# Kernel optimization log

Hardware: AMD Instinct MI355X
Metric: run time of the kernel (lower is better)

The kernel has to match this reference:

```python
import jax, jax.numpy as jnp
import numpy as np

B, H, S, D = 2, 16, 2048, 64
SOFTCLAMP = 50.0


def setup_inputs() -> dict:
    key = jax.random.key(0)
    kq, kk, kv, km = jax.random.split(key, 4)
    q = jax.random.normal(kq, (B, H, S, D), dtype=jnp.float32)
    k = jax.random.normal(kk, (B, H, S, D), dtype=jnp.float32)
    v = jax.random.normal(kv, (B, H, S, D), dtype=jnp.float32)
    mask = jax.random.randint(km, (B, S), 0, 2).astype(jnp.bool_)
    return {"q": q, "k": k, "v": v, "mask": mask}


def reference(q, k, v, mask):
    scale = q.shape[-1] ** -0.5
    # [b, h, i, j] similarity logits
    sim = jnp.einsum('bhid,bhjd->bhij', q, k) * scale
    # tanh-based logit softclamping (Gemma2-style softcapping)
    sim = jnp.tanh(sim / SOFTCLAMP) * SOFTCLAMP
    mask_value = -jnp.finfo(sim.dtype).max
    sim = jnp.where(mask[:, None, None, :], sim, mask_value)
    attn = jax.nn.softmax(sim, axis=-1)
    out = jnp.einsum('bhij,bhjd->bhid', attn, v)
    return out, attn
```

## Files before the change

### kernel.cpp

```cpp
#include <hip/hip_runtime.h>
#include <hip/hip_bf16.h>

#define B_ 2
#define H_ 16
#define S_ 2048
#define D_ 64
#define PSTR 2056

typedef float f32x4 __attribute__((ext_vector_type(4)));
typedef short s16x8 __attribute__((ext_vector_type(8)));

__device__ __forceinline__ short f2bf(float f) {
  unsigned u = __float_as_uint(f);
  u += 0x7FFFu + ((u >> 16) & 1u);
  return (short)(u >> 16);
}
__device__ __forceinline__ float bf2f(short s) {
  return __uint_as_float(((unsigned)(unsigned short)s) << 16);
}

__global__ __launch_bounds__(256) void prep_qk(const float* __restrict__ q,
                                               const float* __restrict__ k,
                                               short* __restrict__ qbf,
                                               short* __restrict__ kbf) {
  size_t i = ((size_t)blockIdx.x * 256 + threadIdx.x) * 8;
  const f32x4* qa = (const f32x4*)(q + i);
  const f32x4* ka = (const f32x4*)(k + i);
  f32x4 a0 = __builtin_nontemporal_load(qa);
  f32x4 a1 = __builtin_nontemporal_load(qa + 1);
  f32x4 b0 = __builtin_nontemporal_load(ka);
  f32x4 b1 = __builtin_nontemporal_load(ka + 1);
  s16x8 oq, ok;
  #pragma unroll
  for (int e = 0; e < 4; ++e) {
    oq[e] = f2bf(a0[e]); oq[4 + e] = f2bf(a1[e]);
    ok[e] = f2bf(b0[e]); ok[4 + e] = f2bf(b1[e]);
  }
  *(s16x8*)(qbf + i) = oq;
  *(s16x8*)(kbf + i) = ok;
}

__global__ __launch_bounds__(256) void prep_v(const float* __restrict__ v,
                                              short* __restrict__ vt) {
  __shared__ float tile[64][65];
  const int tid = threadIdx.x;
  const int j0 = blockIdx.x * 64;
  const int bh = blockIdx.y;
  const float* vh = v + (size_t)bh * S_ * D_;
  #pragma unroll
  for (int it = 0; it < 16; ++it) {
    int idx = it * 256 + tid;
    int row = idx >> 6, col = idx & 63;
    tile[row][col] = __builtin_nontemporal_load(&vh[(size_t)(j0 + row) * D_ + col]);
  }
  __syncthreads();
  short* vth = vt + (size_t)bh * D_ * S_;
  #pragma unroll
  for (int it = 0; it < 16; ++it) {
    int idx = it * 256 + tid;
    int d = idx >> 6, jj = idx & 63;
    vth[(size_t)d * S_ + j0 + jj] = f2bf(tile[jj][d]);
  }
}

template <bool PRE>
__global__ __launch_bounds__(512, 4) void attend_kernel(
    const float* __restrict__ q, const float* __restrict__ k,
    const float* __restrict__ v, const int* __restrict__ mask,
    const short* __restrict__ qbf, const short* __restrict__ kbf,
    const short* __restrict__ vt,
    float* __restrict__ out, float* __restrict__ attn) {
  __shared__ short ps[16 * PSTR];
  __shared__ float ls_rs[8][16];
  __shared__ float ls_rinv[16];

  const int tid  = threadIdx.x;
  const int wv   = tid >> 6;
  const int lane = tid & 63;
  const int lg   = lane >> 4;
  const int li   = lane & 15;

  const int q0 = blockIdx.x * 16;
  const int bh = blockIdx.y;
  const int b  = bh >> 4;
  const int* mrow = mask + (size_t)b * S_;

  s16x8 qf[2];
  if constexpr (PRE) {
    const short* qr = qbf + ((size_t)bh * S_ + q0 + li) * D_ + lg * 8;
    qf[0] = *(const s16x8*)qr;
    qf[1] = *(const s16x8*)(qr + 32);
  } else {
    const float* qr = q + ((size_t)bh * S_ + q0 + li) * D_ + lg * 8;
    #pragma unroll
    for (int ks = 0; ks < 2; ++ks)
      #pragma unroll
      for (int e = 0; e < 8; ++e) qf[ks][e] = f2bf(qr[ks * 32 + e]);
  }

  float rs[4] = {0.f, 0.f, 0.f, 0.f};

  for (int c = wv; c < S_ / 64; c += 8) {
    const int jc = c * 64;
    f32x4 acc[4];
    #pragma unroll
    for (int n = 0; n < 4; ++n) acc[n] = (f32x4){0.f, 0.f, 0.f, 0.f};

    #pragma unroll
    for (int n = 0; n < 4; ++n) {
      if constexpr (PRE) {
        const short* kr = kbf + ((size_t)bh * S_ + jc + n * 16 + li) * D_ + lg * 8;
        acc[n] = __builtin_amdgcn_mfma_f32_16x16x32_bf16(qf[0], *(const s16x8*)kr, acc[n], 0, 0, 0);
        acc[n] = __builtin_amdgcn_mfma_f32_16x16x32_bf16(qf[1], *(const s16x8*)(kr + 32), acc[n], 0, 0, 0);
      } else {
        const float* kr = k + ((size_t)bh * S_ + jc + n * 16 + li) * D_ + lg * 8;
        s16x8 kf0, kf1;
        #pragma unroll
        for (int e = 0; e < 8; ++e) { kf0[e] = f2bf(kr[e]); kf1[e] = f2bf(kr[32 + e]); }
        acc[n] = __builtin_amdgcn_mfma_f32_16x16x32_bf16(qf[0], kf0, acc[n], 0, 0, 0);
        acc[n] = __builtin_amdgcn_mfma_f32_16x16x32_bf16(qf[1], kf1, acc[n], 0, 0, 0);
      }
    }

    #pragma unroll
    for (int n = 0; n < 4; ++n) {
      const int j = jc + n * 16 + li;
      const bool keep = mrow[j] != 0;
      #pragma unroll
      for (int r = 0; r < 4; ++r) {
        float s = acc[n][r] * 0.125f;
        float t = exp2f(s * 0.057707802f);
        float p = exp2f(-144.269504f * __builtin_amdgcn_rcpf(t + 1.f));
        p = keep ? p : 0.f;
        rs[r] += p;
        ps[(lg * 4 + r) * PSTR + j] = f2bf(p);
      }
    }
  }

  #pragma unroll
  for (int r = 0; r < 4; ++r) {
    #pragma unroll
    for (int m = 1; m < 16; m <<= 1) rs[r] += __shfl_xor(rs[r], m, 64);
  }
  if (li == 0) {
    #pragma unroll
    for (int r = 0; r < 4; ++r) ls_rs[wv][lg * 4 + r] = rs[r];
  }
  __syncthreads();
  if (tid < 16) {
    float ssum = 0.f;
    #pragma unroll
    for (int w = 0; w < 8; ++w) ssum += ls_rs[w][tid];
    ls_rinv[tid] = (ssum > 0.f) ? 1.f / ssum : 0.f;
  }
  __syncthreads();

  if (wv < 4) {
    float* abase = attn + ((size_t)bh * S_ + q0) * S_;
    #pragma unroll 4
    for (int qq = 0; qq < 16; ++qq) {
      const float ri = ls_rinv[qq];
      s16x8 pv = *(const s16x8*)&ps[qq * PSTR + tid * 8];
      f32x4 a0, a1;
      a0[0] = bf2f(pv[0]) * ri; a0[1] = bf2f(pv[1]) * ri;
      a0[2] = bf2f(pv[2]) * ri; a0[3] = bf2f(pv[3]) * ri;
      a1[0] = bf2f(pv[4]) * ri; a1[1] = bf2f(pv[5]) * ri;
      a1[2] = bf2f(pv[6]) * ri; a1[3] = bf2f(pv[7]) * ri;
      f32x4* ap = (f32x4*)(abase + (size_t)qq * S_ + tid * 8);
      __builtin_nontemporal_store(a0, ap);
      __builtin_nontemporal_store(a1, ap + 1);
    }
  } else {
    const int d0 = (wv - 4) * 16;
    f32x4 oa = (f32x4){0.f, 0.f, 0.f, 0.f};
    f32x4 ob = (f32x4){0.f, 0.f, 0.f, 0.f};
    if constexpr (PRE) {
      const short* vrow = vt + ((size_t)bh * D_ + d0 + li) * S_;
      #pragma unroll 2
      for (int jc = 0; jc < S_; jc += 64) {
        s16x8 pa0 = *(const s16x8*)&ps[li * PSTR + jc + lg * 8];
        s16x8 pa1 = *(const s16x8*)&ps[li * PSTR + jc + 32 + lg * 8];
        s16x8 vb0 = *(const s16x8*)(vrow + jc + lg * 8);
        s16x8 vb1 = *(const s16x8*)(vrow + jc + 32 + lg * 8);
        oa = __builtin_amdgcn_mfma_f32_16x16x32_bf16(pa0, vb0, oa, 0, 0, 0);
        ob = __builtin_amdgcn_mfma_f32_16x16x32_bf16(pa1, vb1, ob, 0, 0, 0);
      }
    } else {
      const float* vp0 = v + (size_t)bh * S_ * D_ + d0 + li;
      for (int jc = 0; jc < S_; jc += 32) {
        s16x8 pa = *(const s16x8*)&ps[li * PSTR + jc + lg * 8];
        s16x8 vb;
        const float* vp = vp0 + (size_t)(jc + lg * 8) * D_;
        #pragma unroll
        for (int e = 0; e < 8; ++e) vb[e] = f2bf(vp[(size_t)e * D_]);
        oa = __builtin_amdgcn_mfma_f32_16x16x32_bf16(pa, vb, oa, 0, 0, 0);
      }
    }
    #pragma unroll
    for (int r = 0; r < 4; ++r) {
      const int qq = lg * 4 + r;
      out[((size_t)bh * S_ + q0 + qq) * D_ + d0 + li] = (oa[r] + ob[r]) * ls_rinv[qq];
    }
  }
}

extern "C" void kernel_launch(void* const* d_in, const int* in_sizes, int n_in,
                              void* d_out, int out_size, void* d_ws, size_t ws_size,
                              hipStream_t stream) {
  const float* q = (const float*)d_in[0];
  const float* k = (const float*)d_in[1];
  const float* v = (const float*)d_in[2];
  const int* mask = (const int*)d_in[3];

  float* out  = (float*)d_out;
  const size_t nel = (size_t)B_ * H_ * S_ * D_;
  float* attn = out + nel;

  dim3 grid(S_ / 16, B_ * H_);
  const size_t need = nel * 2 * 3;

  if (ws_size >= need) {
    short* qbf = (short*)d_ws;
    short* kbf = qbf + nel;
    short* vtp = kbf + nel;
    prep_qk<<<(int)(nel / (256 * 8)), 256, 0, stream>>>(q, k, qbf, kbf);
    prep_v<<<dim3(S_ / 64, B_ * H_), 256, 0, stream>>>(v, vtp);
    attend_kernel<true><<<grid, 512, 0, stream>>>(q, k, v, mask, qbf, kbf, vtp, out, attn);
  } else {
    attend_kernel<false><<<grid, 512, 0, stream>>>(q, k, v, mask, nullptr, nullptr, nullptr, out, attn);
  }
}
```

Baseline: 332.5 us.

## Fuse PV matmul into the QK loop with per-wave LDS buffers and register-held probabilities

Each wave now computes P·V for its own 64-key chunks right after the softmax numerators, using a small per-wave LDS staging buffer instead of a full 16x2048 probability tile. Partial outputs are reduced across waves through LDS. Probabilities are kept packed in registers and written to attn after normalization, so all 8 waves share the store work. This cuts LDS use to raise occupancy and spreads the attn writes and PV work evenly, at the cost of more registers and a cross-wave reduction. The attn stores are now scalar and strided per lane rather than vectorized.

```diff
diff --git a/kernel.cpp b/kernel.cpp
--- a/kernel.cpp
+++ b/kernel.cpp
@@ -5,7 +5,8 @@
 #define H_ 16
 #define S_ 2048
 #define D_ 64
-#define PSTR 2056
+#define BUFSTR 72
+#define BUFSZ (16 * BUFSTR)
 
 typedef float f32x4 __attribute__((ext_vector_type(4)));
 typedef short s16x8 __attribute__((ext_vector_type(8)));
@@ -64,13 +65,13 @@
 }
 
 template <bool PRE>
-__global__ __launch_bounds__(512, 4) void attend_kernel(
+__global__ __launch_bounds__(512, 4) void attend_fused(
     const float* __restrict__ q, const float* __restrict__ k,
     const float* __restrict__ v, const int* __restrict__ mask,
     const short* __restrict__ qbf, const short* __restrict__ kbf,
     const short* __restrict__ vt,
     float* __restrict__ out, float* __restrict__ attn) {
-  __shared__ short ps[16 * PSTR];
+  __shared__ float pvred[8][16][64];
   __shared__ float ls_rs[8][16];
   __shared__ float ls_rinv[16];
 
@@ -85,40 +86,45 @@
   const int b  = bh >> 4;
   const int* mrow = mask + (size_t)b * S_;
 
-  s16x8 qf[2];
+  short* myb = (short*)pvred + wv * BUFSZ;
+
+  s16x8 qf0, qf1;
   if constexpr (PRE) {
     const short* qr = qbf + ((size_t)bh * S_ + q0 + li) * D_ + lg * 8;
-    qf[0] = *(const s16x8*)qr;
-    qf[1] = *(const s16x8*)(qr + 32);
+    qf0 = *(const s16x8*)qr;
+    qf1 = *(const s16x8*)(qr + 32);
   } else {
     const float* qr = q + ((size_t)bh * S_ + q0 + li) * D_ + lg * 8;
     #pragma unroll
-    for (int ks = 0; ks < 2; ++ks)
-      #pragma unroll
-      for (int e = 0; e < 8; ++e) qf[ks][e] = f2bf(qr[ks * 32 + e]);
+    for (int e = 0; e < 8; ++e) { qf0[e] = f2bf(qr[e]); qf1[e] = f2bf(qr[32 + e]); }
   }
 
   float rs[4] = {0.f, 0.f, 0.f, 0.f};
-
-  for (int c = wv; c < S_ / 64; c += 8) {
-    const int jc = c * 64;
+  f32x4 pvacc[4];
+  #pragma unroll
+  for (int m = 0; m < 4; ++m) pvacc[m] = (f32x4){0.f, 0.f, 0.f, 0.f};
+  unsigned st[4][4][2];
+
+  #pragma unroll
+  for (int c = 0; c < 4; ++c) {
+    const int jc = c * 512 + wv * 64;
+
     f32x4 acc[4];
     #pragma unroll
     for (int n = 0; n < 4; ++n) acc[n] = (f32x4){0.f, 0.f, 0.f, 0.f};
-
     #pragma unroll
     for (int n = 0; n < 4; ++n) {
       if constexpr (PRE) {
         const short* kr = kbf + ((size_t)bh * S_ + jc + n * 16 + li) * D_ + lg * 8;
-        acc[n] = __builtin_amdgcn_mfma_f32_16x16x32_bf16(qf[0], *(const s16x8*)kr, acc[n], 0, 0, 0);
-        acc[n] = __builtin_amdgcn_mfma_f32_16x16x32_bf16(qf[1], *(const s16x8*)(kr + 32), acc[n], 0, 0, 0);
+        acc[n] = __builtin_amdgcn_mfma_f32_16x16x32_bf16(qf0, *(const s16x8*)kr, acc[n], 0, 0, 0);
+        acc[n] = __builtin_amdgcn_mfma_f32_16x16x32_bf16(qf1, *(const s16x8*)(kr + 32), acc[n], 0, 0, 0);
       } else {
         const float* kr = k + ((size_t)bh * S_ + jc + n * 16 + li) * D_ + lg * 8;
-        s16x8 kf0, kf1;
+        s16x8 k0, k1;
         #pragma unroll
-        for (int e = 0; e < 8; ++e) { kf0[e] = f2bf(kr[e]); kf1[e] = f2bf(kr[32 + e]); }
-        acc[n] = __builtin_amdgcn_mfma_f32_16x16x32_bf16(qf[0], kf0, acc[n], 0, 0, 0);
-        acc[n] = __builtin_amdgcn_mfma_f32_16x16x32_bf16(qf[1], kf1, acc[n], 0, 0, 0);
+        for (int e = 0; e < 8; ++e) { k0[e] = f2bf(kr[e]); k1[e] = f2bf(kr[32 + e]); }
+        acc[n] = __builtin_amdgcn_mfma_f32_16x16x32_bf16(qf0, k0, acc[n], 0, 0, 0);
+        acc[n] = __builtin_amdgcn_mfma_f32_16x16x32_bf16(qf1, k1, acc[n], 0, 0, 0);
       }
     }
 
@@ -126,6 +132,7 @@
     for (int n = 0; n < 4; ++n) {
       const int j = jc + n * 16 + li;
       const bool keep = mrow[j] != 0;
+      unsigned pk0 = 0, pk1 = 0;
       #pragma unroll
       for (int r = 0; r < 4; ++r) {
         float s = acc[n][r] * 0.125f;
@@ -133,7 +140,31 @@
         float p = exp2f(-144.269504f * __builtin_amdgcn_rcpf(t + 1.f));
         p = keep ? p : 0.f;
         rs[r] += p;
-        ps[(lg * 4 + r) * PSTR + j] = f2bf(p);
+        unsigned pb = (unsigned)(unsigned short)f2bf(p);
+        if (r == 0) pk0 = pb;
+        else if (r == 1) pk0 |= pb << 16;
+        else if (r == 2) pk1 = pb;
+        else pk1 |= pb << 16;
+        myb[(lg * 4 + r) * BUFSTR + n * 16 + li] = (short)pb;
+      }
+      st[c][n][0] = pk0;
+      st[c][n][1] = pk1;
+    }
+
+    #pragma unroll
+    for (int ks = 0; ks < 2; ++ks) {
+      s16x8 pa = *(const s16x8*)&myb[li * BUFSTR + ks * 32 + lg * 8];
+      #pragma unroll
+      for (int m = 0; m < 4; ++m) {
+        s16x8 vb;
+        if constexpr (PRE) {
+          vb = *(const s16x8*)(vt + ((size_t)bh * D_ + m * 16 + li) * S_ + jc + ks * 32 + lg * 8);
+        } else {
+          const float* vp = v + (size_t)bh * S_ * D_ + (size_t)(jc + ks * 32 + lg * 8) * D_ + m * 16 + li;
+          #pragma unroll
+          for (int e = 0; e < 8; ++e) vb[e] = f2bf(vp[(size_t)e * D_]);
+        }
+        pvacc[m] = __builtin_amdgcn_mfma_f32_16x16x32_bf16(pa, vb, pvacc[m], 0, 0, 0);
       }
     }
   }
@@ -148,59 +179,49 @@
     for (int r = 0; r < 4; ++r) ls_rs[wv][lg * 4 + r] = rs[r];
   }
   __syncthreads();
+
   if (tid < 16) {
     float ssum = 0.f;
     #pragma unroll
     for (int w = 0; w < 8; ++w) ssum += ls_rs[w][tid];
     ls_rinv[tid] = (ssum > 0.f) ? 1.f / ssum : 0.f;
   }
+  #pragma unroll
+  for (int m = 0; m < 4; ++m)
+    #pragma unroll
+    for (int r = 0; r < 4; ++r)
+      pvred[wv][lg * 4 + r][m * 16 + li] = pvacc[m][r];
   __syncthreads();
 
-  if (wv < 4) {
-    float* abase = attn + ((size_t)bh * S_ + q0) * S_;
-    #pragma unroll 4
-    for (int qq = 0; qq < 16; ++qq) {
-      const float ri = ls_rinv[qq];
-      s16x8 pv = *(const s16x8*)&ps[qq * PSTR + tid * 8];
-      f32x4 a0, a1;
-      a0[0] = bf2f(pv[0]) * ri; a0[1] = bf2f(pv[1]) * ri;
-      a0[2] = bf2f(pv[2]) * ri; a0[3] = bf2f(pv[3]) * ri;
-      a1[0] = bf2f(pv[4]) * ri; a1[1] = bf2f(pv[5]) * ri;
-      a1[2] = bf2f(pv[6]) * ri; a1[3] = bf2f(pv[7]) * ri;
-      f32x4* ap = (f32x4*)(abase + (size_t)qq * S_ + tid * 8);
-      __builtin_nontemporal_store(a0, ap);
-      __builtin_nontemporal_store(a1, ap + 1);
-    }
-  } else {
-    const int d0 = (wv - 4) * 16;
-    f32x4 oa = (f32x4){0.f, 0.f, 0.f, 0.f};
-    f32x4 ob = (f32x4){0.f, 0.f, 0.f, 0.f};
-    if constexpr (PRE) {
-      const short* vrow = vt + ((size_t)bh * D_ + d0 + li) * S_;
-      #pragma unroll 2
-      for (int jc = 0; jc < S_; jc += 64) {
-        s16x8 pa0 = *(const s16x8*)&ps[li * PSTR + jc + lg * 8];
-        s16x8 pa1 = *(const s16x8*)&ps[li * PSTR + jc + 32 + lg * 8];
-        s16x8 vb0 = *(const s16x8*)(vrow + jc + lg * 8);
-        s16x8 vb1 = *(const s16x8*)(vrow + jc + 32 + lg * 8);
-        oa = __builtin_amdgcn_mfma_f32_16x16x32_bf16(pa0, vb0, oa, 0, 0, 0);
-        ob = __builtin_amdgcn_mfma_f32_16x16x32_bf16(pa1, vb1, ob, 0, 0, 0);
-      }
-    } else {
-      const float* vp0 = v + (size_t)bh * S_ * D_ + d0 + li;
-      for (int jc = 0; jc < S_; jc += 32) {
-        s16x8 pa = *(const s16x8*)&ps[li * PSTR + jc + lg * 8];
-        s16x8 vb;
-        const float* vp = vp0 + (size_t)(jc + lg * 8) * D_;
-        #pragma unroll
-        for (int e = 0; e < 8; ++e) vb[e] = f2bf(vp[(size_t)e * D_]);
-        oa = __builtin_amdgcn_mfma_f32_16x16x32_bf16(pa, vb, oa, 0, 0, 0);
-      }
-    }
-    #pragma unroll
-    for (int r = 0; r < 4; ++r) {
-      const int qq = lg * 4 + r;
-      out[((size_t)bh * S_ + q0 + qq) * D_ + d0 + li] = (oa[r] + ob[r]) * ls_rinv[qq];
+  #pragma unroll
+  for (int h = 0; h < 2; ++h) {
+    const int idx = h * 512 + tid;
+    const int qq = idx >> 6, d = idx & 63;
+    float ssum = 0.f;
+    #pragma unroll
+    for (int w = 0; w < 8; ++w) ssum += pvred[w][qq][d];
+    out[((size_t)bh * S_ + q0 + qq) * D_ + d] = ssum * ls_rinv[qq];
+  }
+
+  float rinv4[4];
+  #pragma unroll
+  for (int r = 0; r < 4; ++r) rinv4[r] = ls_rinv[lg * 4 + r];
+
+  float* abase = attn + ((size_t)bh * S_ + q0 + lg * 4) * S_;
+  #pragma unroll
+  for (int c = 0; c < 4; ++c) {
+    const int jc = c * 512 + wv * 64;
+    #pragma unroll
+    for (int n = 0; n < 4; ++n) {
+      const int j = jc + n * 16 + li;
+      #pragma unroll
+      for (int rr = 0; rr < 2; ++rr) {
+        unsigned pk = st[c][n][rr];
+        float p0 = bf2f((short)(pk & 0xFFFFu)) * rinv4[2 * rr];
+        float p1 = bf2f((short)(pk >> 16)) * rinv4[2 * rr + 1];
+        __builtin_nontemporal_store(p0, abase + (size_t)(2 * rr) * S_ + j);
+        __builtin_nontemporal_store(p1, abase + (size_t)(2 * rr + 1) * S_ + j);
+      }
     }
   }
 }
@@ -226,8 +247,8 @@
     short* vtp = kbf + nel;
     prep_qk<<<(int)(nel / (256 * 8)), 256, 0, stream>>>(q, k, qbf, kbf);
     prep_v<<<dim3(S_ / 64, B_ * H_), 256, 0, stream>>>(v, vtp);
-    attend_kernel<true><<<grid, 512, 0, stream>>>(q, k, v, mask, qbf, kbf, vtp, out, attn);
+    attend_fused<true><<<grid, 512, 0, stream>>>(q, k, v, mask, qbf, kbf, vtp, out, attn);
   } else {
-    attend_kernel<false><<<grid, 512, 0, stream>>>(q, k, v, mask, nullptr, nullptr, nullptr, out, attn);
-  }
-}
+    attend_fused<false><<<grid, 512, 0, stream>>>(q, k, v, mask, nullptr, nullptr, nullptr, out, attn);
+  }
+}
```

New measurement: 390.8 us. +17.5%, slower.
